# Optimization experiments

Hardware: AMD Instinct MI355X
Metric: run time of the kernel (lower is better)

The kernel has to match this reference:

```python
import jax, jax.numpy as jnp
import numpy as np

N_NODES = 50000
N_EDGES = 800000
IN_CH = 64
HEADS = 8
OUT_CH = 8
LEAKY_ALPHA = 0.3  # Keras LeakyReLU default


def setup_inputs() -> dict:
    key = jax.random.key(0)
    k1, k2, k3, k4, k5 = jax.random.split(key, 5)
    h = jax.random.normal(k1, (N_NODES, IN_CH), dtype=jnp.float32)
    W = jax.random.normal(k2, (2 * IN_CH, HEADS * OUT_CH), dtype=jnp.float32) * 0.1
    a = jax.random.normal(k3, (1, HEADS * OUT_CH), dtype=jnp.float32) * 0.1
    src = jax.random.randint(k4, (N_EDGES,), 0, N_NODES, dtype=jnp.int32)
    tgt = jax.random.randint(k5, (N_EDGES,), 0, N_NODES, dtype=jnp.int32)
    return {"h": h, "W": W, "a": a, "src": src, "tgt": tgt}


def reference(h, W, a, src, tgt):
    # h: [N, C]; W: [2C, H*D]; a: [1, H*D]; src/tgt: [E]
    N = h.shape[0]
    hi = h[src]                                   # [E, C] gather source feats
    hj = h[tgt]                                   # [E, C] gather target feats
    hij = jnp.concatenate([hi, hj], axis=-1)      # [E, 2C]
    e = jax.nn.leaky_relu(hij @ W, negative_slope=LEAKY_ALPHA)  # [E, H*D]
    # (dropout omitted: eval mode)
    e = e * a                                     # broadcast attention vector
    e = e.reshape(-1, HEADS, OUT_CH).sum(axis=-1)  # [E, H] per-head logits
    # segment softmax over target nodes (numerically stable)
    m = jax.ops.segment_max(e, tgt, num_segments=N)   # [N, H]
    ex = jnp.exp(e - m[tgt])                          # [E, H]
    s = jax.ops.segment_sum(ex, tgt, num_segments=N)  # [N, H]
    att = ex / s[tgt]                                 # [E, H]
    # weight source features per head (in_channel == head*out_channel branch)
    msg = hi.reshape(-1, HEADS, OUT_CH) * att[:, :, None]  # [E, H, D]
    out = jax.ops.segment_sum(msg.reshape(-1, HEADS * OUT_CH), tgt, num_segments=N)
    return out  # [N, H*D]
```

## Files before the change

kernel.cpp:

```cpp
#include <hip/hip_runtime.h>
#include <hip/hip_fp16.h>
#include <math.h>

#define ALPHA 0.3f
#define MAXDEG 64
#define LOG2E 1.44269504088896f
#define UVOFF (64 * 68 + 4)

__device__ __forceinline__ unsigned int pack2(float u, float hv) {
    __half2 p = __floats2half2_rn(u, hv);
    unsigned int w;
    __builtin_memcpy(&w, &p, 4);
    return w;
}

__device__ __forceinline__ float2 unpack2(unsigned int w) {
    __half2 p;
    __builtin_memcpy(&p, &w, 4);
    return __half22float2(p);
}

__device__ __forceinline__ float dpp_sum8(float z) {
    int t;
    t = __builtin_amdgcn_mov_dpp(__float_as_int(z), 0xB1, 0xF, 0xF, true);
    z += __int_as_float(t);
    t = __builtin_amdgcn_mov_dpp(__float_as_int(z), 0x4E, 0xF, 0xF, true);
    z += __int_as_float(t);
    t = __builtin_amdgcn_mov_dpp(__float_as_int(z), 0x141, 0xF, 0xF, true);
    z += __int_as_float(t);
    return z;
}

__global__ __launch_bounds__(256) void k_uv(const float* __restrict__ h,
                                            const float* __restrict__ W,
                                            unsigned int* __restrict__ g,
                                            float* __restrict__ vbuf,
                                            int* __restrict__ cursor, int N) {
    __shared__ float Ws[UVOFF + 64 * 68];
    const int t = threadIdx.x;
    const int gidx = blockIdx.x * 256 + t;
    if (gidx < N) cursor[gidx] = 0;

    for (int i = t; i < 128 * 64; i += 256) {
        const int row = i >> 6, col = i & 63;
        const int idx = (row < 64) ? (row * 68 + col) : (UVOFF + (row - 64) * 68 + col);
        Ws[idx] = W[i];
    }
    __syncthreads();

    const int nb = blockIdx.x * 64;
    const int kk = t & 15;
    const int gn = t >> 4;
    const int colbase = (kk * 8) & 63;
    const int wbase   = (kk < 8) ? 0 : UVOFF;

    int nidx[4];
#pragma unroll
    for (int i = 0; i < 4; ++i) {
        int n = nb + gn * 4 + i;
        nidx[i] = (n < N) ? n : (N - 1);
    }

    float acc[4][8];
#pragma unroll
    for (int i = 0; i < 4; ++i)
#pragma unroll
        for (int j = 0; j < 8; ++j) acc[i][j] = 0.0f;

    for (int c4 = 0; c4 < 64; c4 += 4) {
        float hh[4][4];
#pragma unroll
        for (int i = 0; i < 4; ++i) {
            const float4 tv = *(const float4*)&h[(size_t)nidx[i] * 64 + c4];
            hh[i][0] = tv.x; hh[i][1] = tv.y; hh[i][2] = tv.z; hh[i][3] = tv.w;
        }
#pragma unroll
        for (int cc = 0; cc < 4; ++cc) {
            const float* wrow = &Ws[wbase + (c4 + cc) * 68 + colbase];
            const float4 w0 = *(const float4*)(wrow);
            const float4 w1 = *(const float4*)(wrow + 4);
            const float wv[8] = {w0.x, w0.y, w0.z, w0.w, w1.x, w1.y, w1.z, w1.w};
#pragma unroll
            for (int i = 0; i < 4; ++i)
#pragma unroll
                for (int j = 0; j < 8; ++j) acc[i][j] += hh[i][cc] * wv[j];
        }
    }

#pragma unroll
    for (int i = 0; i < 4; ++i) {
        const int n = nb + gn * 4 + i;
        if (n >= N) continue;
        if (kk < 8) {
            const float4 h0 = *(const float4*)&h[(size_t)n * 64 + colbase];
            const float4 h1 = *(const float4*)&h[(size_t)n * 64 + colbase + 4];
            const float hv[8] = {h0.x, h0.y, h0.z, h0.w, h1.x, h1.y, h1.z, h1.w};
            unsigned int w[8];
#pragma unroll
            for (int j = 0; j < 8; ++j) w[j] = pack2(acc[i][j], hv[j]);
            uint4 w0 = {w[0], w[1], w[2], w[3]};
            uint4 w1 = {w[4], w[5], w[6], w[7]};
            *(uint4*)&g[(size_t)n * 64 + colbase]     = w0;
            *(uint4*)&g[(size_t)n * 64 + colbase + 4] = w1;
        } else {
            float4 o0 = {acc[i][0], acc[i][1], acc[i][2], acc[i][3]};
            float4 o1 = {acc[i][4], acc[i][5], acc[i][6], acc[i][7]};
            *(float4*)&vbuf[(size_t)n * 64 + colbase]     = o0;
            *(float4*)&vbuf[(size_t)n * 64 + colbase + 4] = o1;
        }
    }
}

__global__ __launch_bounds__(256) void k_fill(const int* __restrict__ src,
                                              const int* __restrict__ tgt,
                                              int* __restrict__ cursor,
                                              unsigned short* __restrict__ srcs, int E) {
    const int q = blockIdx.x * 256 + threadIdx.x;
    const int e = q * 4;
    if (e + 4 <= E) {
        const int4 s4 = *(const int4*)(src + e);
        const int4 t4 = *(const int4*)(tgt + e);
        int p;
        p = atomicAdd(&cursor[t4.x], 1); if (p < MAXDEG) srcs[(size_t)t4.x * MAXDEG + p] = (unsigned short)s4.x;
        p = atomicAdd(&cursor[t4.y], 1); if (p < MAXDEG) srcs[(size_t)t4.y * MAXDEG + p] = (unsigned short)s4.y;
        p = atomicAdd(&cursor[t4.z], 1); if (p < MAXDEG) srcs[(size_t)t4.z * MAXDEG + p] = (unsigned short)s4.z;
        p = atomicAdd(&cursor[t4.w], 1); if (p < MAXDEG) srcs[(size_t)t4.w * MAXDEG + p] = (unsigned short)s4.w;
    } else {
        for (int i = e; i < E; ++i) {
            const int ti = tgt[i];
            const int p = atomicAdd(&cursor[ti], 1);
            if (p < MAXDEG) srcs[(size_t)ti * MAXDEG + p] = (unsigned short)src[i];
        }
    }
}

__global__ __launch_bounds__(256) void k_node(const unsigned int* __restrict__ g,
                                              const float* __restrict__ vbuf,
                                              const float* __restrict__ a,
                                              const int* __restrict__ cnt,
                                              const unsigned short* __restrict__ srcs,
                                              float* __restrict__ out, int N) {
    const int wid  = (blockIdx.x * 256 + threadIdx.x) >> 6;
    const int lane = threadIdx.x & 63;
    if (wid >= N) return;

    const float v_l = vbuf[(size_t)wid * 64 + lane];
    const float a_l = a[lane] * LOG2E;
    const int num = min(cnt[wid], MAXDEG);
    const int beg = wid * MAXDEG;

    float l_run = 0.0f, acc = 0.0f;

    int k = 0;
    for (; k + 8 <= num; k += 8) {
        const ushort4 sa = *(const ushort4*)(srcs + beg + k);
        const ushort4 sb = *(const ushort4*)(srcs + beg + k + 4);
        unsigned int w[8];
        w[0] = g[(size_t)sa.x * 64 + lane];
        w[1] = g[(size_t)sa.y * 64 + lane];
        w[2] = g[(size_t)sa.z * 64 + lane];
        w[3] = g[(size_t)sa.w * 64 + lane];
        w[4] = g[(size_t)sb.x * 64 + lane];
        w[5] = g[(size_t)sb.y * 64 + lane];
        w[6] = g[(size_t)sb.z * 64 + lane];
        w[7] = g[(size_t)sb.w * 64 + lane];
#pragma unroll
        for (int j = 0; j < 8; ++j) {
            const float2 f = unpack2(w[j]);
            const float q = f.x + v_l;
            float z = fmaxf(q, q * ALPHA) * a_l;
            z = dpp_sum8(z);
            const float p = __builtin_amdgcn_exp2f(z);
            l_run += p;
            acc = fmaf(f.y, p, acc);
        }
    }
    for (; k < num; ++k) {
        const int s = srcs[beg + k];
        const float2 f = unpack2(g[(size_t)s * 64 + lane]);
        const float q = f.x + v_l;
        float z = fmaxf(q, q * ALPHA) * a_l;
        z = dpp_sum8(z);
        const float p = __builtin_amdgcn_exp2f(z);
        l_run += p;
        acc = fmaf(f.y, p, acc);
    }

    out[(size_t)wid * 64 + lane] = (num > 0) ? (acc / l_run) : 0.0f;
}

extern "C" void kernel_launch(void* const* d_in, const int* in_sizes, int n_in,
                              void* d_out, int out_size, void* d_ws, size_t ws_size,
                              hipStream_t stream) {
    const float* h   = (const float*)d_in[0];
    const float* W   = (const float*)d_in[1];
    const float* a   = (const float*)d_in[2];
    const int*   src = (const int*)d_in[3];
    const int*   tgt = (const int*)d_in[4];
    float* out = (float*)d_out;

    const int N = in_sizes[0] / 64;
    const int E = in_sizes[3];

    unsigned int*   g      = (unsigned int*)d_ws;
    float*          vbuf   = (float*)(g + (size_t)N * 64);
    int*            cursor = (int*)(vbuf + (size_t)N * 64);
    unsigned short* srcs   = (unsigned short*)(cursor + N);

    k_uv<<<(N + 63) / 64, 256, 0, stream>>>(h, W, g, vbuf, cursor, N);
    k_fill<<<(E / 4 + 255) / 256, 256, 0, stream>>>(src, tgt, cursor, srcs, E);
    k_node<<<((size_t)N * 64 + 255) / 256, 256, 0, stream>>>(g, vbuf, a, cursor, srcs, out, N);
}
```

Baseline: 106.6 us.

## Partition CSR fill by target residue and add 4-wide tail in node kernel

After: 99.37 us. -6.8%, faster.

```diff
diff --git a/kernel.cpp b/kernel.cpp
--- a/kernel.cpp
+++ b/kernel.cpp
@@ -6,6 +6,7 @@
 #define MAXDEG 64
 #define LOG2E 1.44269504088896f
 #define UVOFF (64 * 68 + 4)
+#define NSLICE 128
 
 __device__ __forceinline__ unsigned int pack2(float u, float hv) {
     __half2 p = __floats2half2_rn(u, hv);
@@ -115,21 +116,28 @@
                                               const int* __restrict__ tgt,
                                               int* __restrict__ cursor,
                                               unsigned short* __restrict__ srcs, int E) {
-    const int q = blockIdx.x * 256 + threadIdx.x;
-    const int e = q * 4;
-    if (e + 4 <= E) {
-        const int4 s4 = *(const int4*)(src + e);
-        const int4 t4 = *(const int4*)(tgt + e);
-        int p;
-        p = atomicAdd(&cursor[t4.x], 1); if (p < MAXDEG) srcs[(size_t)t4.x * MAXDEG + p] = (unsigned short)s4.x;
-        p = atomicAdd(&cursor[t4.y], 1); if (p < MAXDEG) srcs[(size_t)t4.y * MAXDEG + p] = (unsigned short)s4.y;
-        p = atomicAdd(&cursor[t4.z], 1); if (p < MAXDEG) srcs[(size_t)t4.z * MAXDEG + p] = (unsigned short)s4.z;
-        p = atomicAdd(&cursor[t4.w], 1); if (p < MAXDEG) srcs[(size_t)t4.w * MAXDEG + p] = (unsigned short)s4.w;
-    } else {
-        for (int i = e; i < E; ++i) {
+    const int p  = blockIdx.x & 7;
+    const int sl = blockIdx.x >> 3;
+    const int Q  = E >> 2;
+    const int per = (Q + NSLICE - 1) / NSLICE;
+    const int q0 = sl * per;
+    const int q1 = min(q0 + per, Q);
+
+    for (int q = q0 + (int)threadIdx.x; q < q1; q += 256) {
+        const int4 s4 = ((const int4*)src)[q];
+        const int4 t4 = ((const int4*)tgt)[q];
+        if ((t4.x & 7) == p) { const int pos = atomicAdd(&cursor[t4.x], 1); if (pos < MAXDEG) srcs[(size_t)t4.x * MAXDEG + pos] = (unsigned short)s4.x; }
+        if ((t4.y & 7) == p) { const int pos = atomicAdd(&cursor[t4.y], 1); if (pos < MAXDEG) srcs[(size_t)t4.y * MAXDEG + pos] = (unsigned short)s4.y; }
+        if ((t4.z & 7) == p) { const int pos = atomicAdd(&cursor[t4.z], 1); if (pos < MAXDEG) srcs[(size_t)t4.z * MAXDEG + pos] = (unsigned short)s4.z; }
+        if ((t4.w & 7) == p) { const int pos = atomicAdd(&cursor[t4.w], 1); if (pos < MAXDEG) srcs[(size_t)t4.w * MAXDEG + pos] = (unsigned short)s4.w; }
+    }
+    if (sl == 0) {
+        for (int i = (Q << 2) + (int)threadIdx.x; i < E; i += 256) {
             const int ti = tgt[i];
-            const int p = atomicAdd(&cursor[ti], 1);
-            if (p < MAXDEG) srcs[(size_t)ti * MAXDEG + p] = (unsigned short)src[i];
+            if ((ti & 7) == p) {
+                const int pos = atomicAdd(&cursor[ti], 1);
+                if (pos < MAXDEG) srcs[(size_t)ti * MAXDEG + pos] = (unsigned short)src[i];
+            }
         }
     }
 }
@@ -175,6 +183,25 @@
             acc = fmaf(f.y, p, acc);
         }
     }
+    if (k + 4 <= num) {
+        const ushort4 sa = *(const ushort4*)(srcs + beg + k);
+        unsigned int w[4];
+        w[0] = g[(size_t)sa.x * 64 + lane];
+        w[1] = g[(size_t)sa.y * 64 + lane];
+        w[2] = g[(size_t)sa.z * 64 + lane];
+        w[3] = g[(size_t)sa.w * 64 + lane];
+#pragma unroll
+        for (int j = 0; j < 4; ++j) {
+            const float2 f = unpack2(w[j]);
+            const float q = f.x + v_l;
+            float z = fmaxf(q, q * ALPHA) * a_l;
+            z = dpp_sum8(z);
+            const float p = __builtin_amdgcn_exp2f(z);
+            l_run += p;
+            acc = fmaf(f.y, p, acc);
+        }
+        k += 4;
+    }
     for (; k < num; ++k) {
         const int s = srcs[beg + k];
         const float2 f = unpack2(g[(size_t)s * 64 + lane]);
@@ -208,6 +235,6 @@
     unsigned short* srcs   = (unsigned short*)(cursor + N);
 
     k_uv<<<(N + 63) / 64, 256, 0, stream>>>(h, W, g, vbuf, cursor, N);
-    k_fill<<<(E / 4 + 255) / 256, 256, 0, stream>>>(src, tgt, cursor, srcs, E);
+    k_fill<<<8 * NSLICE, 256, 0, stream>>>(src, tgt, cursor, srcs, E);
     k_node<<<((size_t)N * 64 + 255) / 256, 256, 0, stream>>>(g, vbuf, a, cursor, srcs, out, N);
 }
```
